# Kernel optimization log

Measured on AMD Instinct MI355X. Metric: run time of the kernel, lower is better.

The kernel has to match this reference:

```python
import jax, jax.numpy as jnp
import numpy as np

B, Q, D = 1, 2048, 4096
H, KVH, HD = 32, 8, 128
NS, NW = 4, 2048
G = H // KVH  # num_key_value_groups
ROPE_BASE = 10000.0


def _rope(x, pos):
    # x: [B, h, S, HD], pos: [S] int -> rotary embedding per-segment positions
    d = x.shape[-1]
    inv_freq = 1.0 / (ROPE_BASE ** (jnp.arange(0, d, 2, dtype=jnp.float32) / d))
    ang = pos.astype(jnp.float32)[:, None] * inv_freq[None, :]          # [S, d/2]
    cos = jnp.concatenate([jnp.cos(ang), jnp.cos(ang)], axis=-1)        # [S, d]
    sin = jnp.concatenate([jnp.sin(ang), jnp.sin(ang)], axis=-1)
    x1, x2 = jnp.split(x, 2, axis=-1)
    rot = jnp.concatenate([-x2, x1], axis=-1)
    return x * cos[None, None] + rot * sin[None, None]


def _repeat_kv(x):
    # [B, KVH, S, HD] -> [B, H, S, HD]
    return jnp.repeat(x, G, axis=1)


def setup_inputs() -> dict:
    key = jax.random.key(0)
    ks = jax.random.split(key, 10)
    return {
        'hidden_states': jax.random.normal(ks[0], (B, Q, D), jnp.float32),
        'sink_k': jax.random.normal(ks[1], (B, KVH, NS, HD), jnp.float32),
        'sink_v': jax.random.normal(ks[2], (B, KVH, NS, HD), jnp.float32),
        'win_k': jax.random.normal(ks[3], (B, KVH, NW, HD), jnp.float32),
        'win_v': jax.random.normal(ks[4], (B, KVH, NW, HD), jnp.float32),
        'sink_pos': jnp.arange(NS, dtype=jnp.int64 if jax.config.jax_enable_x64 else jnp.int32),
        'key_pos': jnp.arange(NW) + NS,
        'sink_mask': jnp.zeros((NS,), jnp.float32),   # 1.0 = masked out
        'key_mask': jnp.zeros((NW,), jnp.float32),
        'Wq': jax.random.normal(ks[5], (D, H * HD), jnp.float32) * 0.02,
        'Wk': jax.random.normal(ks[6], (D, KVH * HD), jnp.float32) * 0.02,
        'Wv': jax.random.normal(ks[7], (D, KVH * HD), jnp.float32) * 0.02,
        'Wo': jax.random.normal(ks[8], (H * HD, D), jnp.float32) * 0.02,
    }


def reference(hidden_states, sink_k, sink_v, win_k, win_v, sink_pos, key_pos,
              sink_mask, key_mask, Wq, Wk, Wv, Wo):
    dtype = hidden_states.dtype
    # qkv projections (Llama-style GQA)
    q = (hidden_states @ Wq).reshape(B, Q, H, HD).transpose(0, 2, 1, 3)      # [B,H,Q,HD]
    k = (hidden_states @ Wk).reshape(B, Q, KVH, HD).transpose(0, 2, 1, 3)    # [B,KVH,Q,HD]
    v = (hidden_states @ Wv).reshape(B, Q, KVH, HD).transpose(0, 2, 1, 3)

    # per-segment positions: queries placed after max cached position
    max_pos = jnp.maximum(sink_pos.max(), key_pos.max()) + 1
    query_pos = jnp.arange(Q) + max_pos

    # per-segment RoPE re-computation (cascading cache semantics)
    q = _rope(q, query_pos)
    k_cur = _rope(k, query_pos)          # current keys, rotated at query positions
    sk = _rope(sink_k, sink_pos)         # sink tokens
    wk = _rope(win_k, key_pos)           # cascade window keys

    K = jnp.concatenate([_repeat_kv(sk), _repeat_kv(wk), _repeat_kv(k_cur)], axis=2)  # [B,H,NS+NW+Q,HD]
    V = jnp.concatenate([_repeat_kv(sink_v), _repeat_kv(win_v), _repeat_kv(v)], axis=2)

    scale = 1.0 / np.sqrt(HD)
    scores = jnp.einsum('bhqd,bhkd->bhqk', q, K) * jnp.asarray(scale, dtype)

    # bias: sink/key masks broadcast over queries; causal mask on the query block
    neg = jnp.finfo(dtype).min
    cache_bias = jnp.concatenate([sink_mask, key_mask], axis=0) * neg        # [NS+NW]
    cache_bias = jnp.broadcast_to(cache_bias[None, :], (Q, NS + NW))
    causal = jnp.triu(jnp.full((Q, Q), neg, dtype), k=1)
    bias = jnp.concatenate([cache_bias, causal], axis=1)                     # [Q, NS+NW+Q]

    attn = jax.nn.softmax(scores + bias[None, None], axis=-1)
    out = jnp.einsum('bhqk,bhkd->bhqd', attn, V)                             # [B,H,Q,HD]
    out = out.transpose(0, 2, 1, 3).reshape(B, Q, H * HD)
    return out @ Wo
```

## Files before the change

kernel.cpp:

```cpp
#include <hip/hip_runtime.h>
#include <hip/hip_bf16.h>

typedef __attribute__((ext_vector_type(8))) short short8;
typedef __attribute__((ext_vector_type(4))) float f32x4;
typedef __attribute__((ext_vector_type(4))) unsigned short us4;

#define DEV static __device__ __forceinline__

constexpr int QLEN = 2048;
constexpr int DMODEL = 4096;
constexpr int NHEAD = 32;
constexpr int NKV = 8;
constexpr int HD = 128;
constexpr int NSINK = 4;
constexpr int NWIN = 2048;
constexpr int CUR0 = NSINK + NWIN;
constexpr int KTOT = CUR0 + QLEN;
constexpr int KT_PAD = 4224;
constexpr float LOG2E = 1.4426950408889634f;
constexpr float NEGBIG = -1.0e30f;
constexpr float MSHIFT = 32.0f;
constexpr float QSCALE = 0.08838834764831843f * LOG2E;

DEV unsigned short f2bf(float f) {
  unsigned int u = __float_as_uint(f);
  u += 0x7fffu + ((u >> 16) & 1u);
  return (unsigned short)(u >> 16);
}

DEV unsigned int pk2(float a, float b) {
  __hip_bfloat162 h = __float22bfloat162_rn(make_float2(a, b));
  return *(unsigned int*)&h;
}

DEV void gld16(const void* g, void* l) {
  __builtin_amdgcn_global_load_lds((const __attribute__((address_space(1))) void*)g,
                                   (__attribute__((address_space(3))) void*)l, 16, 0, 0);
}


__global__ void maxpos_kernel(const int* __restrict__ sp, const int* __restrict__ kp,
                              int* __restrict__ outp) {
  __shared__ int red[256];
  int t = threadIdx.x;
  int m = -0x7fffffff;
  for (int i = t; i < NSINK; i += 256) m = max(m, sp[i]);
  for (int i = t; i < NWIN; i += 256) m = max(m, kp[i]);
  red[t] = m;
  __syncthreads();
  for (int s = 128; s > 0; s >>= 1) {
    if (t < s) red[t] = max(red[t], red[t + s]);
    __syncthreads();
  }
  if (t == 0) outp[0] = red[0] + 1;
}

__global__ void bias_kernel(const float* __restrict__ sm, const float* __restrict__ km,
                            float* __restrict__ bias) {
  int kk = blockIdx.x * 256 + threadIdx.x;
  if (kk >= KT_PAD) return;
  float b;
  if (kk < NSINK) b = sm[kk] * NEGBIG * LOG2E - MSHIFT;
  else if (kk < CUR0) b = km[kk - NSINK] * NEGBIG * LOG2E - MSHIFT;
  else if (kk < KTOT) b = -MSHIFT;
  else b = NEGBIG;
  bias[kk] = b;
}

__global__ void postab_kernel(const int* __restrict__ maxp, float2* __restrict__ tab) {
  int q = blockIdx.x, j = threadIdx.x;
  float pos = (float)(maxp[0] + q);
  float invf = exp2f(-(float)(2 * j) * (13.287712379549449f / 128.0f));
  float ang = pos * invf;
  tab[q * 64 + j] = make_float2(__cosf(ang), __sinf(ang));
}

__global__ __launch_bounds__(256) void cvt_kernel(const float* __restrict__ src,
                                                  unsigned short* __restrict__ dst) {
  long i = ((long)blockIdx.x * 256 + threadIdx.x) * 4;
  f32x4 v = *(const f32x4*)(src + i);
  us4 o;
  o[0] = f2bf(v[0]); o[1] = f2bf(v[1]); o[2] = f2bf(v[2]); o[3] = f2bf(v[3]);
  *(us4*)(dst + i) = o;
}

__global__ void transpose_all(const float* __restrict__ Wq, const float* __restrict__ Wk,
                              const float* __restrict__ Wv, const float* __restrict__ Wo,
                              unsigned short* __restrict__ WqkvT,
                              unsigned short* __restrict__ WoT) {
  __shared__ float t[32][33];
  int bx = blockIdx.x;
  const float* W; unsigned short* WT; int N; int xl;
  if (bx < 128)      { W = Wq; WT = WqkvT;                   N = 4096; xl = bx; }
  else if (bx < 160) { W = Wk; WT = WqkvT + 4096L * 4096;    N = 1024; xl = bx - 128; }
  else if (bx < 192) { W = Wv; WT = WqkvT + 5120L * 4096;    N = 1024; xl = bx - 160; }
  else               { W = Wo; WT = WoT;                     N = 4096; xl = bx - 192; }
  int n0 = xl * 32, k0 = blockIdx.y * 32;
  int tx = threadIdx.x, ty = threadIdx.y;
  for (int p = 0; p < 4; p++) {
    int k = k0 + ty + p * 8;
    t[ty + p * 8][tx] = W[(long)k * N + n0 + tx];
  }
  __syncthreads();
  for (int p = 0; p < 4; p++) {
    int n = n0 + ty + p * 8;
    WT[(long)n * 4096 + k0 + tx] = f2bf(t[tx][ty + p * 8]);
  }
}

__global__ __launch_bounds__(256) void gemm_bt(const unsigned short* __restrict__ A,
                                               const unsigned short* __restrict__ Bt,
                                               float* __restrict__ C,
                                               int M, int N, int K) {
  __shared__ __align__(16) unsigned short As[128 * 64];
  __shared__ __align__(16) unsigned short Bs[128 * 64];
  int tid = threadIdx.x, lane = tid & 63, w = tid >> 6;
  int m0 = blockIdx.y * 128, n0 = blockIdx.x * 128;
  int wm = w & 1, wn = w >> 1;
  f32x4 z = {0.f, 0.f, 0.f, 0.f};
  f32x4 acc[4][4];
  for (int i = 0; i < 4; i++) for (int j = 0; j < 4; j++) acc[i][j] = z;
  int nK = K >> 6;
  for (int ks = 0; ks < nK; ks++) {
    long k0 = (long)ks << 6;
    for (int t = 0; t < 4; t++) {
      int chunk = w * 4 + t;
      int row = chunk * 8 + (lane >> 3);
      int kbs = (lane & 7) ^ (row & 7);
      gld16(A + ((long)(m0 + row) * K + k0 + kbs * 8), &As[chunk * 512 + lane * 8]);
      gld16(Bt + ((long)(n0 + row) * K + k0 + kbs * 8), &Bs[chunk * 512 + lane * 8]);
    }
    __syncthreads();
    for (int kc = 0; kc < 2; kc++) {
      short8 af[4], bf[4];
      int c = kc * 4 + (lane >> 4);
      for (int i = 0; i < 4; i++) {
        int ra = wm * 64 + i * 16 + (lane & 15);
        af[i] = *(const short8*)&As[ra * 64 + (c ^ (ra & 7)) * 8];
        int rb = wn * 64 + i * 16 + (lane & 15);
        bf[i] = *(const short8*)&Bs[rb * 64 + (c ^ (rb & 7)) * 8];
      }
      for (int i = 0; i < 4; i++)
        for (int j = 0; j < 4; j++)
          acc[i][j] = __builtin_amdgcn_mfma_f32_16x16x32_bf16(af[i], bf[j], acc[i][j], 0, 0, 0);
    }
    __syncthreads();
  }
  for (int i = 0; i < 4; i++) {
    int m = m0 + wm * 64 + i * 16 + ((lane >> 4) << 2);
    for (int j = 0; j < 4; j++) {
      int n = n0 + wn * 64 + j * 16 + (lane & 15);
      float* cp = C + (long)m * N + n;
      for (int r = 0; r < 4; r++) cp[(long)r * N] = acc[i][j][r];
    }
  }
}

__global__ __launch_bounds__(256) void gemm_qkv(const unsigned short* __restrict__ A,
                                                const unsigned short* __restrict__ Bt,
                                                const float2* __restrict__ postab,
                                                unsigned short* __restrict__ Qb,
                                                unsigned short* __restrict__ Kb,
                                                unsigned short* __restrict__ VTb) {
  __shared__ __align__(16) char smem[66 * 512];
  unsigned short* As = (unsigned short*)smem;
  unsigned short* Bs = As + 8192;
  float* Cs = (float*)smem;
  constexpr int K = 4096;
  int tid = threadIdx.x, lane = tid & 63, w = tid >> 6;
  int quad = lane >> 4, l15 = lane & 15;
  int m0 = blockIdx.y * 128, n0 = blockIdx.x * 128;
  int wm = w & 1, wn = w >> 1;
  f32x4 z = {0.f, 0.f, 0.f, 0.f};
  f32x4 acc[4][4];
  for (int i = 0; i < 4; i++) for (int j = 0; j < 4; j++) acc[i][j] = z;
  for (int ks = 0; ks < K / 64; ks++) {
    long k0 = (long)ks << 6;
    for (int t = 0; t < 4; t++) {
      int chunk = w * 4 + t;
      int row = chunk * 8 + (lane >> 3);
      int kbs = (lane & 7) ^ (row & 7);
      gld16(A + ((long)(m0 + row) * K + k0 + kbs * 8), &As[chunk * 512 + lane * 8]);
      gld16(Bt + ((long)(n0 + row) * K + k0 + kbs * 8), &Bs[chunk * 512 + lane * 8]);
    }
    __syncthreads();
    for (int kc = 0; kc < 2; kc++) {
      short8 af[4], bf[4];
      int c = kc * 4 + quad;
      for (int i = 0; i < 4; i++) {
        int ra = wm * 64 + i * 16 + l15;
        af[i] = *(const short8*)&As[ra * 64 + (c ^ (ra & 7)) * 8];
        int rb = wn * 64 + i * 16 + l15;
        bf[i] = *(const short8*)&Bs[rb * 64 + (c ^ (rb & 7)) * 8];
      }
      for (int i = 0; i < 4; i++)
        for (int j = 0; j < 4; j++)
          acc[i][j] = __builtin_amdgcn_mfma_f32_16x16x32_bf16(af[i], bf[j], acc[i][j], 0, 0, 0);
    }
    __syncthreads();
  }

  int nb = blockIdx.x;
  int part = (nb < 32) ? 0 : (nb < 40 ? 1 : 2);
  int hh = (part == 0) ? nb : (part == 1 ? nb - 32 : nb - 40);
  float scale = (part == 0) ? QSCALE : 1.0f;

  for (int pass = 0; pass < 2; pass++) {
    __syncthreads();
    if (wm == pass) {
      for (int i = 0; i < 4; i++)
        for (int j = 0; j < 4; j++)
          for (int r = 0; r < 4; r++)
            Cs[(i * 16 + quad * 4 + r) * 129 + wn * 64 + j * 16 + l15] = acc[i][j][r];
    }
    __syncthreads();
    if (part < 2) {
      if (tid < 128) {
        int r = tid & 63, hf = tid >> 6;
        int query = m0 + pass * 64 + r;
        const float2* tb = postab + query * 64;
        unsigned short* dst = (part == 0)
            ? Qb + ((long)hh * QLEN + query) * HD + hf * 64
            : Kb + ((long)hh * KT_PAD + CUR0 + query) * HD + hf * 64;
        for (int j = 0; j < 64; j += 4) {
          float v[4];
          for (int u = 0; u < 4; u++) {
            float2 cs = tb[j + u];
            int d = hf * 64 + j + u;
            float xa = Cs[r * 129 + d];
            float xb = Cs[r * 129 + (d ^ 64)];
            v[u] = (xa * cs.x + (hf ? xb : -xb) * cs.y) * scale;
          }
          uint2 o4;
          o4.x = pk2(v[0], v[1]);
          o4.y = pk2(v[2], v[3]);
          *(uint2*)(dst + j) = o4;
        }
      }
    } else {
      if (tid < 128) {
        int d = tid;
        unsigned short* dst = VTb + ((long)hh * HD + d) * KT_PAD + CUR0 + m0 + pass * 64;
        for (int m = 0; m < 64; m += 4) {
          uint2 o4;
          o4.x = pk2(Cs[m * 129 + d], Cs[(m + 1) * 129 + d]);
          o4.y = pk2(Cs[(m + 2) * 129 + d], Cs[(m + 3) * 129 + d]);
          *(uint2*)(dst + m) = o4;
        }
      }
    }
  }
}

__global__ void rope_cache(const float* __restrict__ sink_k, const float* __restrict__ win_k,
                           const int* __restrict__ sp, const int* __restrict__ kp,
                           unsigned short* __restrict__ Kb) {
  int s = blockIdx.x, kvh = blockIdx.y, d = threadIdx.x;
  const float* src; int pos;
  if (s < NSINK) { src = sink_k + ((long)kvh * NSINK + s) * HD; pos = sp[s]; }
  else           { src = win_k + ((long)kvh * NWIN + (s - NSINK)) * HD; pos = kp[s - NSINK]; }
  float x = src[d];
  float x2 = src[d ^ 64];
  float rot = (d < 64) ? -x2 : x2;
  int i = d & 63;
  float invf = exp2f(-(float)(2 * i) * (13.287712379549449f / 128.0f));
  float ang = (float)pos * invf;
  float c = __cosf(ang), sn = __sinf(ang);
  Kb[((long)kvh * KT_PAD + s) * HD + d] = f2bf(x * c + rot * sn);
}

__global__ void scatter_cache(const float* __restrict__ sink_v, const float* __restrict__ win_v,
                              unsigned short* __restrict__ VTb) {
  __shared__ float t[32][33];
  int kvh = blockIdx.z, d0 = blockIdx.y * 32;
  const float* src; int S, s0, dstPos0;
  if (blockIdx.x < 64) { src = win_v + (long)kvh * NWIN * HD; S = NWIN; s0 = blockIdx.x * 32; dstPos0 = NSINK; }
  else                 { src = sink_v + (long)kvh * NSINK * HD; S = NSINK; s0 = 0; dstPos0 = 0; }
  int tx = threadIdx.x, ty = threadIdx.y;
  for (int p = 0; p < 4; p++) {
    int s = s0 + ty + p * 8;
    if (s < S) t[ty + p * 8][tx] = src[(long)s * HD + d0 + tx];
  }
  __syncthreads();
  for (int p = 0; p < 4; p++) {
    int d = d0 + ty + p * 8;
    int s = s0 + tx;
    if (s < S)
      VTb[((long)kvh * HD + d) * KT_PAD + dstPos0 + s] = f2bf(t[tx][ty + p * 8]);
  }
}

__global__ void pad_zero(unsigned short* __restrict__ Kb, unsigned short* __restrict__ VTb) {
  int idx = blockIdx.x * 256 + threadIdx.x;
  int total = NKV * (KT_PAD - KTOT) * HD;
  if (idx >= total) return;
  int per = (KT_PAD - KTOT) * HD;
  int kvh = idx / per;
  int rem = idx % per;
  int pos = KTOT + rem / HD;
  int d = rem % HD;
  Kb[((long)kvh * KT_PAD + pos) * HD + d] = 0;
  VTb[((long)kvh * HD + d) * KT_PAD + pos] = 0;
}

DEV void stage_kv(const unsigned short* __restrict__ Kbase,
                  const unsigned short* __restrict__ Vbase, long k0,
                  unsigned short* KtB, unsigned short* VtB, int w, int lane) {
  int quad = lane >> 4, l15 = lane & 15;
  for (int t = 0; t < 4; t++) {
    int chunk = w * 4 + t;
    { int row = chunk * 4 + quad;
      int kbs = l15 ^ (row & 15);
      gld16(Kbase + (k0 + row) * HD + kbs * 8, &KtB[chunk * 512 + lane * 8]); }
    { int row = chunk * 8 + (lane >> 3);
      int kbs = (lane & 7) ^ (row & 7);
      gld16(Vbase + (long)row * KT_PAD + k0 + kbs * 8, &VtB[chunk * 512 + lane * 8]); }
  }
}

__global__ __launch_bounds__(256) void attn_kernel(
    const unsigned short* __restrict__ Qb,
    const unsigned short* __restrict__ Kb,
    const unsigned short* __restrict__ VTb,
    const float* __restrict__ biasArr,
    unsigned short* __restrict__ attnOut) {
  __shared__ __align__(16) unsigned short Kt[2][64 * 128];
  __shared__ __align__(16) unsigned short Vt[2][128 * 64];
  __shared__ __align__(16) unsigned short Pl[4][16 * 72];
  __shared__ float abuf[4][2][16];
  int tid = threadIdx.x, lane = tid & 63, w = tid >> 6;
  int quad = lane >> 4, l15 = lane & 15;
  int hh = blockIdx.x;
  int h = (hh & 7) * 4 + (hh >> 3);
  int kvh = hh & 7;
  int yt = blockIdx.y;
  int qt = (yt < 8) ? yt : (23 - yt);
  int q0 = qt * 128;
  int wq0 = q0 + w * 32;

  short8 qf[2][4];
  for (int g = 0; g < 2; g++)
    for (int kc = 0; kc < 4; kc++) {
      long off = ((long)h * QLEN + wq0 + g * 16 + l15) * HD + kc * 32 + quad * 8;
      qf[g][kc] = *(const short8*)(Qb + off);
    }

  f32x4 z = {0.f, 0.f, 0.f, 0.f};
  f32x4 o[2][8];
  for (int g = 0; g < 2; g++) for (int j = 0; j < 8; j++) o[g][j] = z;
  float lrun[2] = {0.f, 0.f};

  int nsteps = min(KT_PAD / 64, (CUR0 + q0 + 127) / 64 + 1);
  const unsigned short* Kbase = Kb + (long)kvh * KT_PAD * HD;
  const unsigned short* Vbase = VTb + (long)kvh * HD * KT_PAD;

  stage_kv(Kbase, Vbase, 0, Kt[0], Vt[0], w, lane);

  for (int st = 0; st < nsteps; st++) {
    long k0 = (long)st * 64;
    int cur = st & 1;
    __syncthreads();

    f32x4 b4[4];
    for (int t = 0; t < 4; t++)
      b4[t] = *(const f32x4*)&biasArr[k0 + 16 * t + quad * 4];

    if (st + 1 < nsteps)
      stage_kv(Kbase, Vbase, k0 + 64, Kt[cur ^ 1], Vt[cur ^ 1], w, lane);

    const unsigned short* KtB = Kt[cur];
    const unsigned short* VtB = Vt[cur];

    f32x4 stt[2][4];
    for (int g = 0; g < 2; g++) for (int t = 0; t < 4; t++) stt[g][t] = z;
    for (int kc = 0; kc < 4; kc++) {
      for (int t = 0; t < 4; t++) {
        int row = 16 * t + l15;
        short8 kf = *(const short8*)&KtB[row * 128 + (((kc * 4 + quad) ^ (row & 15))) * 8];
        stt[0][t] = __builtin_amdgcn_mfma_f32_16x16x32_bf16(kf, qf[0][kc], stt[0][t], 0, 0, 0);
        stt[1][t] = __builtin_amdgcn_mfma_f32_16x16x32_bf16(kf, qf[1][kc], stt[1][t], 0, 0, 0);
      }
    }

    for (int g = 0; g < 2; g++) {
      if ((int)k0 > wq0 + g * 16 + 15 + CUR0) continue;
      int query = wq0 + g * 16 + l15;
      bool needMask = (int)k0 + 63 > wq0 + g * 16 + CUR0;
      float ps = 0.f;
      if (needMask) {
        for (int t = 0; t < 4; t++) {
          float p[4];
          for (int r = 0; r < 4; r++) {
            int key = (int)k0 + 16 * t + quad * 4 + r;
            float v = stt[g][t][r] + b4[t][r];
            if (key > query + CUR0) v = NEGBIG;
            p[r] = exp2f(v);
            ps += p[r];
          }
          uint2 pw;
          pw.x = pk2(p[0], p[1]);
          pw.y = pk2(p[2], p[3]);
          *(uint2*)&Pl[w][l15 * 72 + 16 * t + quad * 4] = pw;
        }
      } else {
        for (int t = 0; t < 4; t++) {
          float p[4];
          for (int r = 0; r < 4; r++) {
            p[r] = exp2f(stt[g][t][r] + b4[t][r]);
            ps += p[r];
          }
          uint2 pw;
          pw.x = pk2(p[0], p[1]);
          pw.y = pk2(p[2], p[3]);
          *(uint2*)&Pl[w][l15 * 72 + 16 * t + quad * 4] = pw;
        }
      }
      lrun[g] += ps;
      short8 pf[2];
      pf[0] = *(const short8*)&Pl[w][l15 * 72 + 0 * 32 + quad * 8];
      pf[1] = *(const short8*)&Pl[w][l15 * 72 + 1 * 32 + quad * 8];
      for (int c = 0; c < 2; c++) {
        for (int jd = 0; jd < 8; jd++) {
          int row = jd * 16 + l15;
          short8 vf = *(const short8*)&VtB[row * 64 + (((c * 4 + quad) ^ (row & 7))) * 8];
          o[g][jd] = __builtin_amdgcn_mfma_f32_16x16x32_bf16(pf[c], vf, o[g][jd], 0, 0, 0);
        }
      }
    }
  }

  for (int g = 0; g < 2; g++) {
    float l = lrun[g];
    l += __shfl_xor(l, 16, 64);
    l += __shfl_xor(l, 32, 64);
    if (lane < 16) abuf[w][g][lane] = 1.0f / l;
  }
  for (int g = 0; g < 2; g++) {
    f32x4 lv = *(const f32x4*)&abuf[w][g][quad * 4];
    for (int r = 0; r < 4; r++) {
      int qrow = wq0 + g * 16 + quad * 4 + r;
      unsigned short* op = attnOut + (long)qrow * DMODEL + h * HD;
      for (int jd = 0; jd < 8; jd++) op[jd * 16 + l15] = f2bf(o[g][jd][r] * lv[r]);
    }
  }
}

extern "C" void kernel_launch(void* const* d_in, const int* in_sizes, int n_in,
                              void* d_out, int out_size, void* d_ws, size_t ws_size,
                              hipStream_t stream) {
  (void)in_sizes; (void)n_in; (void)out_size; (void)ws_size;
  const float* hidden    = (const float*)d_in[0];
  const float* sink_k    = (const float*)d_in[1];
  const float* sink_v    = (const float*)d_in[2];
  const float* win_k     = (const float*)d_in[3];
  const float* win_v     = (const float*)d_in[4];
  const int*   sink_pos  = (const int*)d_in[5];
  const int*   key_pos   = (const int*)d_in[6];
  const float* sink_mask = (const float*)d_in[7];
  const float* key_mask  = (const float*)d_in[8];
  const float* Wq = (const float*)d_in[9];
  const float* Wk = (const float*)d_in[10];
  const float* Wv = (const float*)d_in[11];
  const float* Wo = (const float*)d_in[12];
  float* out = (float*)d_out;

  char* ws = (char*)d_ws;
  unsigned short* hidB  = (unsigned short*)(ws + 0);
  unsigned short* attn  = (unsigned short*)(ws + 0);
  unsigned short* WoT   = (unsigned short*)(ws + 16777216L);
  unsigned short* WqkvT = (unsigned short*)(ws + 50331648L);
  unsigned short* Qb    = (unsigned short*)(ws + 100663296L);
  unsigned short* Kb    = (unsigned short*)(ws + 117440512L);
  unsigned short* VTb   = (unsigned short*)(ws + 126091264L);
  float2* postab        = (float2*)(ws + 134742016L);
  float* bias           = (float*)(ws + 135790592L);
  int* maxp             = (int*)(ws + 135807488L);

  maxpos_kernel<<<1, 256, 0, stream>>>(sink_pos, key_pos, maxp);
  bias_kernel<<<(KT_PAD + 255) / 256, 256, 0, stream>>>(sink_mask, key_mask, bias);
  postab_kernel<<<QLEN, 64, 0, stream>>>(maxp, postab);
  cvt_kernel<<<(QLEN * DMODEL / 4) / 256, 256, 0, stream>>>(hidden, hidB);
  transpose_all<<<dim3(320, 128), dim3(32, 8), 0, stream>>>(Wq, Wk, Wv, Wo, WqkvT, WoT);

  gemm_qkv<<<dim3(48, 16), 256, 0, stream>>>(hidB, WqkvT, postab, Qb, Kb, VTb);

  rope_cache<<<dim3(CUR0, NKV), 128, 0, stream>>>(sink_k, win_k, sink_pos, key_pos, Kb);
  scatter_cache<<<dim3(65, 4, NKV), dim3(32, 8), 0, stream>>>(sink_v, win_v, VTb);
  pad_zero<<<(NKV * (KT_PAD - KTOT) * HD + 255) / 256, 256, 0, stream>>>(Kb, VTb);

  attn_kernel<<<dim3(32, 16), 256, 0, stream>>>(Qb, Kb, VTb, bias, attn);

  gemm_bt<<<dim3(32, 16), 256, 0, stream>>>(attn, WoT, out, QLEN, DMODEL, DMODEL);
}
```

Measured before the change: 766.7 us.

## Use 8 waves of 16 queries per attention block, MFMA row sums, swizzled P

The attention block grows from 4 to 8 waves, each owning 16 query rows instead of 32, so K/V staging per wave is halved and register pressure drops enough to request higher occupancy. Softmax row sums are now accumulated with an MFMA against a ones vector instead of scalar adds plus a cross-lane reduction. The P staging buffer uses an XOR swizzle in place of padding to avoid LDS bank conflicts, and s_setprio is raised around the MFMA sections. The cost is more waves sharing the same K/V tiles per block, which adds barrier participants, plus one extra MFMA per chunk.

Result: faster. 693.6 us (-9.5%).

```diff
diff --git a/kernel.cpp b/kernel.cpp
--- a/kernel.cpp
+++ b/kernel.cpp
@@ -307,8 +307,8 @@
                   const unsigned short* __restrict__ Vbase, long k0,
                   unsigned short* KtB, unsigned short* VtB, int w, int lane) {
   int quad = lane >> 4, l15 = lane & 15;
-  for (int t = 0; t < 4; t++) {
-    int chunk = w * 4 + t;
+  for (int t = 0; t < 2; t++) {
+    int chunk = w * 2 + t;
     { int row = chunk * 4 + quad;
       int kbs = l15 ^ (row & 15);
       gld16(Kbase + (k0 + row) * HD + kbs * 8, &KtB[chunk * 512 + lane * 8]); }
@@ -318,7 +318,7 @@
   }
 }
 
-__global__ __launch_bounds__(256) void attn_kernel(
+__global__ __launch_bounds__(512, 4) void attn_kernel(
     const unsigned short* __restrict__ Qb,
     const unsigned short* __restrict__ Kb,
     const unsigned short* __restrict__ VTb,
@@ -326,8 +326,7 @@
     unsigned short* __restrict__ attnOut) {
   __shared__ __align__(16) unsigned short Kt[2][64 * 128];
   __shared__ __align__(16) unsigned short Vt[2][128 * 64];
-  __shared__ __align__(16) unsigned short Pl[4][16 * 72];
-  __shared__ float abuf[4][2][16];
+  __shared__ __align__(16) unsigned short Pl[8][1024];
   int tid = threadIdx.x, lane = tid & 63, w = tid >> 6;
   int quad = lane >> 4, l15 = lane & 15;
   int hh = blockIdx.x;
@@ -336,19 +335,20 @@
   int yt = blockIdx.y;
   int qt = (yt < 8) ? yt : (23 - yt);
   int q0 = qt * 128;
-  int wq0 = q0 + w * 32;
-
-  short8 qf[2][4];
-  for (int g = 0; g < 2; g++)
-    for (int kc = 0; kc < 4; kc++) {
-      long off = ((long)h * QLEN + wq0 + g * 16 + l15) * HD + kc * 32 + quad * 8;
-      qf[g][kc] = *(const short8*)(Qb + off);
-    }
+  int wq0 = q0 + w * 16;
+
+  short8 qf[4];
+  for (int kc = 0; kc < 4; kc++) {
+    long off = ((long)h * QLEN + wq0 + l15) * HD + kc * 32 + quad * 8;
+    qf[kc] = *(const short8*)(Qb + off);
+  }
+  short8 ones;
+  for (int i = 0; i < 8; i++) ones[i] = (short)0x3F80;
 
   f32x4 z = {0.f, 0.f, 0.f, 0.f};
-  f32x4 o[2][8];
-  for (int g = 0; g < 2; g++) for (int j = 0; j < 8; j++) o[g][j] = z;
-  float lrun[2] = {0.f, 0.f};
+  f32x4 o[8];
+  for (int j = 0; j < 8; j++) o[j] = z;
+  f32x4 lacc = z;
 
   int nsteps = min(KT_PAD / 64, (CUR0 + q0 + 127) / 64 + 1);
   const unsigned short* Kbase = Kb + (long)kvh * KT_PAD * HD;
@@ -356,6 +356,10 @@
 
   stage_kv(Kbase, Vbase, 0, Kt[0], Vt[0], w, lane);
 
+  char* PlW = (char*)&Pl[w][0];
+  int pwbase = l15 * 128;
+  int pxor = (l15 & 7) << 4;
+
   for (int st = 0; st < nsteps; st++) {
     long k0 = (long)st * 64;
     int cur = st & 1;
@@ -371,77 +375,67 @@
     const unsigned short* KtB = Kt[cur];
     const unsigned short* VtB = Vt[cur];
 
-    f32x4 stt[2][4];
-    for (int g = 0; g < 2; g++) for (int t = 0; t < 4; t++) stt[g][t] = z;
+    f32x4 stt[4];
+    for (int t = 0; t < 4; t++) stt[t] = z;
+    __builtin_amdgcn_s_setprio(1);
     for (int kc = 0; kc < 4; kc++) {
       for (int t = 0; t < 4; t++) {
         int row = 16 * t + l15;
         short8 kf = *(const short8*)&KtB[row * 128 + (((kc * 4 + quad) ^ (row & 15))) * 8];
-        stt[0][t] = __builtin_amdgcn_mfma_f32_16x16x32_bf16(kf, qf[0][kc], stt[0][t], 0, 0, 0);
-        stt[1][t] = __builtin_amdgcn_mfma_f32_16x16x32_bf16(kf, qf[1][kc], stt[1][t], 0, 0, 0);
-      }
-    }
-
-    for (int g = 0; g < 2; g++) {
-      if ((int)k0 > wq0 + g * 16 + 15 + CUR0) continue;
-      int query = wq0 + g * 16 + l15;
-      bool needMask = (int)k0 + 63 > wq0 + g * 16 + CUR0;
-      float ps = 0.f;
+        stt[t] = __builtin_amdgcn_mfma_f32_16x16x32_bf16(kf, qf[kc], stt[t], 0, 0, 0);
+      }
+    }
+    __builtin_amdgcn_s_setprio(0);
+
+    if ((int)k0 <= wq0 + 15 + CUR0) {
+      int query = wq0 + l15;
+      bool needMask = (int)k0 + 63 > wq0 + CUR0;
       if (needMask) {
         for (int t = 0; t < 4; t++) {
           float p[4];
           for (int r = 0; r < 4; r++) {
             int key = (int)k0 + 16 * t + quad * 4 + r;
-            float v = stt[g][t][r] + b4[t][r];
+            float v = stt[t][r] + b4[t][r];
             if (key > query + CUR0) v = NEGBIG;
             p[r] = exp2f(v);
-            ps += p[r];
           }
           uint2 pw;
           pw.x = pk2(p[0], p[1]);
           pw.y = pk2(p[2], p[3]);
-          *(uint2*)&Pl[w][l15 * 72 + 16 * t + quad * 4] = pw;
+          *(uint2*)(PlW + (pwbase + ((32 * t + 8 * quad) ^ pxor))) = pw;
         }
       } else {
         for (int t = 0; t < 4; t++) {
           float p[4];
-          for (int r = 0; r < 4; r++) {
-            p[r] = exp2f(stt[g][t][r] + b4[t][r]);
-            ps += p[r];
-          }
+          for (int r = 0; r < 4; r++) p[r] = exp2f(stt[t][r] + b4[t][r]);
           uint2 pw;
           pw.x = pk2(p[0], p[1]);
           pw.y = pk2(p[2], p[3]);
-          *(uint2*)&Pl[w][l15 * 72 + 16 * t + quad * 4] = pw;
+          *(uint2*)(PlW + (pwbase + ((32 * t + 8 * quad) ^ pxor))) = pw;
         }
       }
-      lrun[g] += ps;
       short8 pf[2];
-      pf[0] = *(const short8*)&Pl[w][l15 * 72 + 0 * 32 + quad * 8];
-      pf[1] = *(const short8*)&Pl[w][l15 * 72 + 1 * 32 + quad * 8];
+      pf[0] = *(const short8*)(PlW + (pwbase + ((16 * quad) ^ pxor)));
+      pf[1] = *(const short8*)(PlW + (pwbase + ((64 + 16 * quad) ^ pxor)));
+      __builtin_amdgcn_s_setprio(1);
       for (int c = 0; c < 2; c++) {
+        lacc = __builtin_amdgcn_mfma_f32_16x16x32_bf16(pf[c], ones, lacc, 0, 0, 0);
         for (int jd = 0; jd < 8; jd++) {
           int row = jd * 16 + l15;
           short8 vf = *(const short8*)&VtB[row * 64 + (((c * 4 + quad) ^ (row & 7))) * 8];
-          o[g][jd] = __builtin_amdgcn_mfma_f32_16x16x32_bf16(pf[c], vf, o[g][jd], 0, 0, 0);
+          o[jd] = __builtin_amdgcn_mfma_f32_16x16x32_bf16(pf[c], vf, o[jd], 0, 0, 0);
         }
       }
-    }
-  }
-
-  for (int g = 0; g < 2; g++) {
-    float l = lrun[g];
-    l += __shfl_xor(l, 16, 64);
-    l += __shfl_xor(l, 32, 64);
-    if (lane < 16) abuf[w][g][lane] = 1.0f / l;
-  }
-  for (int g = 0; g < 2; g++) {
-    f32x4 lv = *(const f32x4*)&abuf[w][g][quad * 4];
-    for (int r = 0; r < 4; r++) {
-      int qrow = wq0 + g * 16 + quad * 4 + r;
-      unsigned short* op = attnOut + (long)qrow * DMODEL + h * HD;
-      for (int jd = 0; jd < 8; jd++) op[jd * 16 + l15] = f2bf(o[g][jd][r] * lv[r]);
-    }
+      __builtin_amdgcn_s_setprio(0);
+    }
+  }
+
+  f32x4 linv;
+  for (int r = 0; r < 4; r++) linv[r] = 1.0f / lacc[r];
+  for (int r = 0; r < 4; r++) {
+    int qrow = wq0 + quad * 4 + r;
+    unsigned short* op = attnOut + (long)qrow * DMODEL + h * HD;
+    for (int jd = 0; jd < 8; jd++) op[jd * 16 + l15] = f2bf(o[jd][r] * linv[r]);
   }
 }
 
@@ -488,7 +482,7 @@
   scatter_cache<<<dim3(65, 4, NKV), dim3(32, 8), 0, stream>>>(sink_v, win_v, VTb);
   pad_zero<<<(NKV * (KT_PAD - KTOT) * HD + 255) / 256, 256, 0, stream>>>(Kb, VTb);
 
-  attn_kernel<<<dim3(32, 16), 256, 0, stream>>>(Qb, Kb, VTb, bias, attn);
+  attn_kernel<<<dim3(32, 16), 512, 0, stream>>>(Qb, Kb, VTb, bias, attn);
 
   gemm_bt<<<dim3(32, 16), 256, 0, stream>>>(attn, WoT, out, QLEN, DMODEL, DMODEL);
 }
```
